# Kernel optimization log

Hardware: AMD Instinct MI355X
Metric: run time of the kernel (lower is better)

## Reference

```python
import jax, jax.numpy as jnp
import numpy as np

E, T, D_IN, D_H = 8, 2048, 2048, 5632


def setup_inputs() -> dict:
    key = jax.random.key(0)
    kx, kg, kd, ku = jax.random.split(key, 4)
    scale = 0.02  # init_std-like scaling for weights
    return {
        "x": jax.random.normal(kx, (E, T, D_IN), dtype=jnp.float32),
        "gate_proj": jax.random.normal(kg, (E, D_IN, D_H), dtype=jnp.float32) * scale,
        "down_proj": jax.random.normal(kd, (E, D_IN, D_H), dtype=jnp.float32) * scale,
        "up_proj": jax.random.normal(ku, (E, D_H, D_IN), dtype=jnp.float32) * scale,
        "tokens_per_expert": T,
    }


def reference(x, gate_proj, down_proj, up_proj, tokens_per_expert):
    # ep_size=1: dispatch/combine are identity. Grouped SwiGLU per expert.
    # x: [E, T, d_in]; gate/down: [E, d_in, d_h]; up: [E, d_h, d_in]
    g = jnp.einsum('etd,edh->eth', x, gate_proj)
    u = jnp.einsum('etd,edh->eth', x, down_proj)
    h = jax.nn.silu(g) * u  # [E, T, d_h]
    out = jnp.einsum('eth,ehd->etd', h, up_proj)  # [E, T, d_in]
    return out
```

## Files before the change

### kernel.cpp

```cpp
#include <hip/hip_runtime.h>
#include <hip/hip_bf16.h>


#define NEXP 8
#define TT   2048
#define DIN  2048
#define DH   5632
#define KP   2080

using short8 = __attribute__((ext_vector_type(8))) short;
using f32x4  = __attribute__((ext_vector_type(4))) float;

static __device__ __forceinline__ unsigned short f2bf(float f) {
    unsigned int i = __float_as_uint(f);
    return (unsigned short)((i + 0x7FFFu + ((i >> 16) & 1u)) >> 16);
}
static __device__ __forceinline__ void gld16(const void* g, void* l) {
    __builtin_amdgcn_global_load_lds(
        (const __attribute__((address_space(1))) void*)g,
        (__attribute__((address_space(3))) void*)l, 16, 0, 0);
}

__global__ __launch_bounds__(512, 2) void gemm_gu(
    const unsigned short* __restrict__ Xb,
    const unsigned short* __restrict__ Wgt,
    const unsigned short* __restrict__ Wdt,
    unsigned short* __restrict__ Hb)
{
    __shared__ __align__(16) unsigned short lds[81920];

    const int tid  = threadIdx.x;
    const int wave = tid >> 6, lane = tid & 63;
    const int l15 = lane & 15, l4 = lane >> 4;
    const int wr = wave >> 2, wc = wave & 3;

    const int bid = blockIdx.x;
    const int e   = bid & 7;
    const int cu  = bid >> 3;
    const int m0  = (cu & 7) * 256;
    const int nb  = cu >> 3;

    const unsigned short* Ae = Xb + (size_t)e * TT * KP;
    unsigned short* He = Hb + (size_t)e * TT * DH;

    const int c0 = tid, c1 = 512 + tid;
    const int cs0 = c0 ^ ((c0 >> 3) & 7), cs1 = c1 ^ ((c1 >> 3) & 7);
    const int row0 = cs0 >> 3, col0 = (cs0 & 7) * 8;
    const int row1 = cs1 >> 3, col1 = (cs1 & 7) * 8;

    int ibA[4][2], ibB[2][2];
#pragma unroll
    for (int s = 0; s < 4; ++s)
#pragma unroll
        for (int ks = 0; ks < 2; ++ks) {
            const int r = wr * 64 + s * 16 + l15;
            ibA[s][ks] = (r * 128 + ks * 64 + l4 * 16) ^ ((r & 7) << 4);
        }
#pragma unroll
    for (int s = 0; s < 2; ++s)
#pragma unroll
        for (int ks = 0; ks < 2; ++ks) {
            const int r = wc * 32 + s * 16 + l15;
            ibB[s][ks] = (r * 128 + ks * 64 + l4 * 16) ^ ((r & 7) << 4);
        }

    f32x4 acc[8][4] = {};
    short8 Aq[4][2], Gq[2][2], Dq[2][2];

    char* ldsb = (char*)lds;
    auto stageA = [&](int ro, int kk, int so) {
        gld16(Ae + (size_t)(m0 + ro + row0) * KP + (kk + col0), ldsb + so + wave * 1024);
        gld16(Ae + (size_t)(m0 + ro + row1) * KP + (kk + col1), ldsb + so + 8192 + wave * 1024);
    };
    auto stageW = [&](const unsigned short* p, int kk, int so) {
        gld16(p + (size_t)row0 * KP + (kk + col0), ldsb + so + wave * 1024);
        gld16(p + (size_t)row1 * KP + (kk + col1), ldsb + so + 8192 + wave * 1024);
    };
    auto w10 = [](int x) { return x >= 10 ? x - 10 : x; };

    const size_t NSTEP = (size_t)512 * KP;
    const unsigned short* Gc = Wgt + (size_t)e * DH * KP + (size_t)(nb * 128) * KP;
    const unsigned short* Dc = Wdt + (size_t)e * DH * KP + (size_t)(nb * 128) * KP;

    stageA(0, 0, 0 << 14);  stageW(Gc, 0, 1 << 14);  stageW(Dc, 0, 2 << 14);  stageA(128, 0, 3 << 14);
    stageA(0, 64, 4 << 14); stageW(Gc, 64, 5 << 14); stageW(Dc, 64, 6 << 14);
    asm volatile("s_waitcnt vmcnt(6)" ::: "memory");
    asm volatile("s_barrier" ::: "memory");

    const char* ldsc = (const char*)lds;
    int q = 0;
    for (int i = 0; i < 11; ++i) {
        const unsigned short* Gn = Gc + NSTEP;
        const unsigned short* Dn = Dc + NSTEP;
        for (int t = 0; t < 32; ++t) {
            const int g = (i << 5) + t;
            const int sA0 = q << 14;
            const int sG  = w10(q + 1) << 14;
            const int sD  = w10(q + 2) << 14;
            const int sA1 = w10(q + 3) << 14;
            const int stA1 = w10(q + 7) << 14;
            const int stA0 = w10(q + 8) << 14;
            const int stG  = w10(q + 9) << 14;
            const int stD  = sA0;

#pragma unroll
            for (int s = 0; s < 4; ++s) {
                Aq[s][0] = *(const short8*)(ldsc + sA0 + ibA[s][0]);
                Aq[s][1] = *(const short8*)(ldsc + sA0 + ibA[s][1]);
            }
#pragma unroll
            for (int s = 0; s < 2; ++s) {
                Gq[s][0] = *(const short8*)(ldsc + sG + ibB[s][0]);
                Gq[s][1] = *(const short8*)(ldsc + sG + ibB[s][1]);
                Dq[s][0] = *(const short8*)(ldsc + sD + ibB[s][0]);
                Dq[s][1] = *(const short8*)(ldsc + sD + ibB[s][1]);
            }
            if (i < 10 || t + 1 < 32)
                stageA(128, ((t + 1) & 31) * 64, stA1);
            asm volatile("s_waitcnt lgkmcnt(0)" ::: "memory");
            __builtin_amdgcn_sched_barrier(0);
            __builtin_amdgcn_s_setprio(1);
#pragma unroll
            for (int m = 0; m < 4; ++m)
#pragma unroll
                for (int n = 0; n < 2; ++n) {
                    acc[m][n] = __builtin_amdgcn_mfma_f32_16x16x32_bf16(Aq[m][0], Gq[n][0], acc[m][n], 0, 0, 0);
                    acc[m][n] = __builtin_amdgcn_mfma_f32_16x16x32_bf16(Aq[m][1], Gq[n][1], acc[m][n], 0, 0, 0);
                }
            __builtin_amdgcn_s_setprio(0);
            if (i < 10 || t + 2 < 32)
                stageA(0, ((t + 2) & 31) * 64, stA0);
            __builtin_amdgcn_s_setprio(1);
#pragma unroll
            for (int m = 0; m < 4; ++m)
#pragma unroll
                for (int n = 0; n < 2; ++n) {
                    acc[m][2 + n] = __builtin_amdgcn_mfma_f32_16x16x32_bf16(Aq[m][0], Dq[n][0], acc[m][2 + n], 0, 0, 0);
                    acc[m][2 + n] = __builtin_amdgcn_mfma_f32_16x16x32_bf16(Aq[m][1], Dq[n][1], acc[m][2 + n], 0, 0, 0);
                }
            __builtin_amdgcn_s_setprio(0);
#pragma unroll
            for (int s = 0; s < 4; ++s) {
                Aq[s][0] = *(const short8*)(ldsc + sA1 + ibA[s][0]);
                Aq[s][1] = *(const short8*)(ldsc + sA1 + ibA[s][1]);
            }
            if (i < 10 || t + 2 < 32)
                stageW((t + 2 < 32) ? Gc : Gn, ((t + 2) & 31) * 64, stG);
            asm volatile("s_waitcnt lgkmcnt(0)" ::: "memory");
            __builtin_amdgcn_sched_barrier(0);
            __builtin_amdgcn_s_setprio(1);
#pragma unroll
            for (int m = 0; m < 4; ++m)
#pragma unroll
                for (int n = 0; n < 2; ++n) {
                    acc[4 + m][2 + n] = __builtin_amdgcn_mfma_f32_16x16x32_bf16(Aq[m][0], Dq[n][0], acc[4 + m][2 + n], 0, 0, 0);
                    acc[4 + m][2 + n] = __builtin_amdgcn_mfma_f32_16x16x32_bf16(Aq[m][1], Dq[n][1], acc[4 + m][2 + n], 0, 0, 0);
                }
#pragma unroll
            for (int m = 0; m < 4; ++m)
#pragma unroll
                for (int n = 0; n < 2; ++n) {
                    acc[4 + m][n] = __builtin_amdgcn_mfma_f32_16x16x32_bf16(Aq[m][0], Gq[n][0], acc[4 + m][n], 0, 0, 0);
                    acc[4 + m][n] = __builtin_amdgcn_mfma_f32_16x16x32_bf16(Aq[m][1], Gq[n][1], acc[4 + m][n], 0, 0, 0);
                }
            __builtin_amdgcn_s_setprio(0);
            asm volatile("s_barrier" ::: "memory");
            if (i < 10 || t + 2 < 32)
                stageW((t + 2 < 32) ? Dc : Dn, ((t + 2) & 31) * 64, stD);
            if (g < 350)       asm volatile("s_waitcnt vmcnt(6)" ::: "memory");
            else if (g == 350) asm volatile("s_waitcnt vmcnt(0)" ::: "memory");
            asm volatile("s_barrier" ::: "memory");
            q = w10(q + 4);
        }

        const int n0i = (4 * i + nb) * 128;
#pragma unroll
        for (int fm = 0; fm < 8; ++fm) {
            const int row_b = m0 + (fm >> 2) * 128 + wr * 64 + (fm & 3) * 16 + l4 * 4;
#pragma unroll
            for (int nr = 0; nr < 2; ++nr) {
                const int col = n0i + wc * 32 + nr * 16 + l15;
#pragma unroll
                for (int j = 0; j < 4; ++j) {
                    const float gv = acc[fm][nr][j];
                    const float uv = acc[fm][2 + nr][j];
                    const float h = gv / (1.f + __expf(-gv)) * uv;
                    He[(size_t)(row_b + j) * DH + col] = f2bf(h);
                }
            }
        }
#pragma unroll
        for (int m = 0; m < 8; ++m)
#pragma unroll
            for (int n = 0; n < 4; ++n)
                acc[m][n] = (f32x4){0.f, 0.f, 0.f, 0.f};
        Gc = Gn; Dc = Dn;
    }
}

__global__ __launch_bounds__(512, 2) void gemm_out(
    const unsigned short* __restrict__ Ab,
    const unsigned short* __restrict__ Btb,
    float* __restrict__ Cf)
{
    __shared__ __align__(16) unsigned short lds[81920];

    const int tid  = threadIdx.x;
    const int wave = tid >> 6, lane = tid & 63;
    const int l15 = lane & 15, l4 = lane >> 4;
    const int wr = wave >> 2, wc = wave & 3;

    const int bid = blockIdx.x;
    const int e   = bid & 7;
    const int cu  = bid >> 3;
    const int m0  = (cu & 7) * 256;
    const int nb  = cu >> 3;

    const int N = DIN, K = DH;
    const unsigned short* Ae = Ab + (size_t)e * TT * DH;

    const int c0 = tid, c1 = 512 + tid;
    const int cs0 = c0 ^ ((c0 >> 3) & 7), cs1 = c1 ^ ((c1 >> 3) & 7);
    const int row0 = cs0 >> 3, col0 = (cs0 & 7) * 8;
    const int row1 = cs1 >> 3, col1 = (cs1 & 7) * 8;

    int ibA[4][2], ibB[2][2];
#pragma unroll
    for (int s = 0; s < 4; ++s)
#pragma unroll
        for (int ks = 0; ks < 2; ++ks) {
            const int r = wr * 64 + s * 16 + l15;
            ibA[s][ks] = (r * 128 + ks * 64 + l4 * 16) ^ ((r & 7) << 4);
        }
#pragma unroll
    for (int s = 0; s < 2; ++s)
#pragma unroll
        for (int ks = 0; ks < 2; ++ks) {
            const int r = wc * 32 + s * 16 + l15;
            ibB[s][ks] = (r * 128 + ks * 64 + l4 * 16) ^ ((r & 7) << 4);
        }

    f32x4 acc[8][4] = {};
    short8 Aq[4][2], B0q[2][2], B1q[2][2];

    char* ldsb = (char*)lds;
    auto stageA = [&](int ro, int kk, int so) {
        gld16(Ae + (size_t)(m0 + ro + row0) * K + (kk + col0), ldsb + so + wave * 1024);
        gld16(Ae + (size_t)(m0 + ro + row1) * K + (kk + col1), ldsb + so + 8192 + wave * 1024);
    };
    auto stageB = [&](const unsigned short* base, int co, int kk, int so) {
        gld16(base + (size_t)(co + row0) * K + (kk + col0), ldsb + so + wave * 1024);
        gld16(base + (size_t)(co + row1) * K + (kk + col1), ldsb + so + 8192 + wave * 1024);
    };
    auto w10 = [](int x) { return x >= 10 ? x - 10 : x; };

    const size_t NSTEP = (size_t)1024 * K;
    const unsigned short* Bc = Btb + (size_t)e * DIN * DH + (size_t)(nb * 256) * K;

    stageA(0, 0, 0 << 14); stageB(Bc, 0, 0, 1 << 14); stageB(Bc, 128, 0, 2 << 14); stageA(128, 0, 3 << 14);
    stageA(0, 64, 4 << 14); stageB(Bc, 0, 64, 5 << 14); stageB(Bc, 128, 64, 6 << 14);
    asm volatile("s_waitcnt vmcnt(6)" ::: "memory");
    asm volatile("s_barrier" ::: "memory");

    const char* ldsc = (const char*)lds;
    int q = 0;
    for (int i = 0; i < 2; ++i) {
        const unsigned short* Bn = Bc + NSTEP;
        for (int t = 0; t < 88; ++t) {
            const int g = i * 88 + t;
            const int sA0 = q << 14;
            const int sB0 = w10(q + 1) << 14;
            const int sB1 = w10(q + 2) << 14;
            const int sA1 = w10(q + 3) << 14;
            const int stA1 = w10(q + 7) << 14;
            const int stA0 = w10(q + 8) << 14;
            const int stB0 = w10(q + 9) << 14;
            const int stB1 = sA0;

#pragma unroll
            for (int s = 0; s < 4; ++s) {
                Aq[s][0] = *(const short8*)(ldsc + sA0 + ibA[s][0]);
                Aq[s][1] = *(const short8*)(ldsc + sA0 + ibA[s][1]);
            }
#pragma unroll
            for (int s = 0; s < 2; ++s) {
                B0q[s][0] = *(const short8*)(ldsc + sB0 + ibB[s][0]);
                B0q[s][1] = *(const short8*)(ldsc + sB0 + ibB[s][1]);
                B1q[s][0] = *(const short8*)(ldsc + sB1 + ibB[s][0]);
                B1q[s][1] = *(const short8*)(ldsc + sB1 + ibB[s][1]);
            }
            {
                const int tt = t + 1;
                if (i < 1 || tt < 88)
                    stageA(128, (tt >= 88 ? tt - 88 : tt) * 64, stA1);
            }
            asm volatile("s_waitcnt lgkmcnt(0)" ::: "memory");
            __builtin_amdgcn_sched_barrier(0);
            __builtin_amdgcn_s_setprio(1);
#pragma unroll
            for (int m = 0; m < 4; ++m)
#pragma unroll
                for (int n = 0; n < 2; ++n) {
                    acc[m][n] = __builtin_amdgcn_mfma_f32_16x16x32_bf16(Aq[m][0], B0q[n][0], acc[m][n], 0, 0, 0);
                    acc[m][n] = __builtin_amdgcn_mfma_f32_16x16x32_bf16(Aq[m][1], B0q[n][1], acc[m][n], 0, 0, 0);
                }
            __builtin_amdgcn_s_setprio(0);
            {
                const int tt = t + 2;
                if (i < 1 || tt < 88)
                    stageA(0, (tt >= 88 ? tt - 88 : tt) * 64, stA0);
            }
            __builtin_amdgcn_s_setprio(1);
#pragma unroll
            for (int m = 0; m < 4; ++m)
#pragma unroll
                for (int n = 0; n < 2; ++n) {
                    acc[m][2 + n] = __builtin_amdgcn_mfma_f32_16x16x32_bf16(Aq[m][0], B1q[n][0], acc[m][2 + n], 0, 0, 0);
                    acc[m][2 + n] = __builtin_amdgcn_mfma_f32_16x16x32_bf16(Aq[m][1], B1q[n][1], acc[m][2 + n], 0, 0, 0);
                }
            __builtin_amdgcn_s_setprio(0);
#pragma unroll
            for (int s = 0; s < 4; ++s) {
                Aq[s][0] = *(const short8*)(ldsc + sA1 + ibA[s][0]);
                Aq[s][1] = *(const short8*)(ldsc + sA1 + ibA[s][1]);
            }
            {
                const int tt = t + 2;
                if (i < 1 || tt < 88)
                    stageB((tt >= 88 ? Bn : Bc), 0, (tt >= 88 ? tt - 88 : tt) * 64, stB0);
            }
            asm volatile("s_waitcnt lgkmcnt(0)" ::: "memory");
            __builtin_amdgcn_sched_barrier(0);
            __builtin_amdgcn_s_setprio(1);
#pragma unroll
            for (int m = 0; m < 4; ++m)
#pragma unroll
                for (int n = 0; n < 2; ++n) {
                    acc[4 + m][2 + n] = __builtin_amdgcn_mfma_f32_16x16x32_bf16(Aq[m][0], B1q[n][0], acc[4 + m][2 + n], 0, 0, 0);
                    acc[4 + m][2 + n] = __builtin_amdgcn_mfma_f32_16x16x32_bf16(Aq[m][1], B1q[n][1], acc[4 + m][2 + n], 0, 0, 0);
                }
#pragma unroll
            for (int m = 0; m < 4; ++m)
#pragma unroll
                for (int n = 0; n < 2; ++n) {
                    acc[4 + m][n] = __builtin_amdgcn_mfma_f32_16x16x32_bf16(Aq[m][0], B0q[n][0], acc[4 + m][n], 0, 0, 0);
                    acc[4 + m][n] = __builtin_amdgcn_mfma_f32_16x16x32_bf16(Aq[m][1], B0q[n][1], acc[4 + m][n], 0, 0, 0);
                }
            __builtin_amdgcn_s_setprio(0);
            asm volatile("s_barrier" ::: "memory");
            {
                const int tt = t + 2;
                if (i < 1 || tt < 88)
                    stageB((tt >= 88 ? Bn : Bc), 128, (tt >= 88 ? tt - 88 : tt) * 64, stB1);
            }
            if (g < 174)       asm volatile("s_waitcnt vmcnt(6)" ::: "memory");
            else if (g == 174) asm volatile("s_waitcnt vmcnt(0)" ::: "memory");
            asm volatile("s_barrier" ::: "memory");
            q = w10(q + 4);
        }

        const int n0i = (4 * i + nb) * 256;
        float* Ce = Cf + (size_t)e * TT * DIN;
#pragma unroll
        for (int fm = 0; fm < 8; ++fm) {
            const int row_b = (fm >> 2) * 128 + wr * 64 + (fm & 3) * 16 + l4 * 4;
#pragma unroll
            for (int fn = 0; fn < 4; ++fn) {
                const int col = n0i + (fn >> 1) * 128 + wc * 32 + (fn & 1) * 16 + l15;
#pragma unroll
                for (int j = 0; j < 4; ++j)
                    Ce[(size_t)(m0 + row_b + j) * N + col] = acc[fm][fn][j];
            }
        }
#pragma unroll
        for (int m = 0; m < 8; ++m)
#pragma unroll
            for (int n = 0; n < 4; ++n)
                acc[m][n] = (f32x4){0.f, 0.f, 0.f, 0.f};
        Bc = Bn;
    }
}

__global__ __launch_bounds__(256) void transpose_f32_bf16(
    const float* __restrict__ in, unsigned short* __restrict__ out,
    int R, int C, int opitch, size_t ies, size_t oes)
{
    in  += (size_t)blockIdx.z * ies;
    out += (size_t)blockIdx.z * oes;
    __shared__ unsigned short t[64][65];
    const int tid = threadIdx.x;
    const int lr = tid >> 4, lc = (tid & 15) * 4;
    const int r0 = blockIdx.y * 64, c0 = blockIdx.x * 64;
#pragma unroll
    for (int i = 0; i < 4; ++i) {
        const int row = lr + i * 16;
        const float4 v = *(const float4*)(in + (size_t)(r0 + row) * C + c0 + lc);
        t[row][lc + 0] = f2bf(v.x); t[row][lc + 1] = f2bf(v.y);
        t[row][lc + 2] = f2bf(v.z); t[row][lc + 3] = f2bf(v.w);
    }
    __syncthreads();
#pragma unroll
    for (int i = 0; i < 4; ++i) {
        const int crow = lr + i * 16;
        ushort4 wv;
        wv.x = t[lc + 0][crow]; wv.y = t[lc + 1][crow];
        wv.z = t[lc + 2][crow]; wv.w = t[lc + 3][crow];
        *(ushort4*)(out + (size_t)(c0 + crow) * opitch + r0 + lc) = wv;
    }
}

__global__ __launch_bounds__(256) void conv_pad_f32_bf16(
    const float* __restrict__ in, unsigned short* __restrict__ out, int n8)
{
    int i = blockIdx.x * 256 + threadIdx.x;
    const int stride = gridDim.x * 256;
    for (; i < n8; i += stride) {
        const int row = i >> 8;
        const int col = (i & 255) * 8;
        const float4 v0 = *(const float4*)(in + (size_t)row * DIN + col);
        const float4 v1 = *(const float4*)(in + (size_t)row * DIN + col + 4);
        ushort4 a, b;
        a.x = f2bf(v0.x); a.y = f2bf(v0.y); a.z = f2bf(v0.z); a.w = f2bf(v0.w);
        b.x = f2bf(v1.x); b.y = f2bf(v1.y); b.z = f2bf(v1.z); b.w = f2bf(v1.w);
        *(ushort4*)(out + (size_t)row * KP + col) = a;
        *(ushort4*)(out + (size_t)row * KP + col + 4) = b;
    }
}

extern "C" void kernel_launch(void* const* d_in, const int* in_sizes, int n_in,
                              void* d_out, int out_size, void* d_ws, size_t ws_size,
                              hipStream_t stream)
{
    const float* x  = (const float*)d_in[0];
    const float* wg = (const float*)d_in[1];
    const float* wd = (const float*)d_in[2];
    const float* wu = (const float*)d_in[3];
    float* out = (float*)d_out;

    const size_t XSZ = (size_t)TT * KP;
    const size_t WPSZ = (size_t)DH * KP;
    const size_t WSZ = (size_t)DIN * DH;
    unsigned short* xb  = (unsigned short*)d_ws;
    unsigned short* wgt = xb  + (size_t)NEXP * XSZ;
    unsigned short* wdt = wgt + (size_t)NEXP * WPSZ;
    unsigned short* hb  = wdt + (size_t)NEXP * WPSZ;

    conv_pad_f32_bf16<<<4096, 256, 0, stream>>>(x, xb, NEXP * TT * (DIN / 8));
    transpose_f32_bf16<<<dim3(DH / 64, DIN / 64, NEXP), 256, 0, stream>>>(
        wg, wgt, DIN, DH, KP, WSZ, WPSZ);
    transpose_f32_bf16<<<dim3(DH / 64, DIN / 64, NEXP), 256, 0, stream>>>(
        wd, wdt, DIN, DH, KP, WSZ, WPSZ);
    gemm_gu<<<256, 512, 0, stream>>>(xb, wgt, wdt, hb);
    transpose_f32_bf16<<<dim3(DIN / 64, DH / 64, NEXP), 256, 0, stream>>>(
        wu, wgt, DH, DIN, DH, WSZ, WSZ);
    gemm_out<<<256, 512, 0, stream>>>(hb, wgt, out);
}
```

Baseline: 1.324 ms.

## Load weight fragments directly from global into registers, stage only activations in LDS

Both GEMM kernels stop staging the weight (B) tiles through LDS. Each wave now reads its own weight fragments straight from global memory into registers, while only the activation tile goes through a smaller triple-buffered LDS ring with a single barrier per step. This cuts LDS footprint, LDS traffic and barriers per K-step. In exchange, weight fragments are no longer shared across waves through LDS, so each weight line is fetched by several waves via cache, and global load latency is exposed unless it overlaps with the MFMAs.

```diff
diff --git a/kernel.cpp b/kernel.cpp
--- a/kernel.cpp
+++ b/kernel.cpp
@@ -27,7 +27,7 @@
     const unsigned short* __restrict__ Wdt,
     unsigned short* __restrict__ Hb)
 {
-    __shared__ __align__(16) unsigned short lds[81920];
+    __shared__ __align__(16) unsigned short lds[49152];
 
     const int tid  = threadIdx.x;
     const int wave = tid >> 6, lane = tid & 63;
@@ -40,15 +40,18 @@
     const int m0  = (cu & 7) * 256;
     const int nb  = cu >> 3;
 
-    const unsigned short* Ae = Xb + (size_t)e * TT * KP;
+    const unsigned short* Ae = Xb + (size_t)e * TT * KP + (size_t)m0 * KP;
     unsigned short* He = Hb + (size_t)e * TT * DH;
 
     const int c0 = tid, c1 = 512 + tid;
     const int cs0 = c0 ^ ((c0 >> 3) & 7), cs1 = c1 ^ ((c1 >> 3) & 7);
     const int row0 = cs0 >> 3, col0 = (cs0 & 7) * 8;
     const int row1 = cs1 >> 3, col1 = (cs1 & 7) * 8;
-
-    int ibA[4][2], ibB[2][2];
+    const size_t loff0 = (size_t)row0 * KP + col0;
+    const size_t loff1 = (size_t)row1 * KP + col1;
+    const int wvoff = wave * 1024;
+
+    int ibA[4][2];
 #pragma unroll
     for (int s = 0; s < 4; ++s)
 #pragma unroll
@@ -56,121 +59,110 @@
             const int r = wr * 64 + s * 16 + l15;
             ibA[s][ks] = (r * 128 + ks * 64 + l4 * 16) ^ ((r & 7) << 4);
         }
-#pragma unroll
-    for (int s = 0; s < 2; ++s)
-#pragma unroll
-        for (int ks = 0; ks < 2; ++ks) {
+
+    const size_t NSTEP = (size_t)512 * KP;
+    const unsigned short* gR[2];
+    const unsigned short* dR[2];
+    {
+        const unsigned short* Gb = Wgt + (size_t)e * DH * KP + (size_t)(nb * 128) * KP;
+        const unsigned short* Db = Wdt + (size_t)e * DH * KP + (size_t)(nb * 128) * KP;
+#pragma unroll
+        for (int s = 0; s < 2; ++s) {
             const int r = wc * 32 + s * 16 + l15;
-            ibB[s][ks] = (r * 128 + ks * 64 + l4 * 16) ^ ((r & 7) << 4);
-        }
+            gR[s] = Gb + (size_t)r * KP + l4 * 8;
+            dR[s] = Db + (size_t)r * KP + l4 * 8;
+        }
+    }
 
     f32x4 acc[8][4] = {};
     short8 Aq[4][2], Gq[2][2], Dq[2][2];
 
     char* ldsb = (char*)lds;
-    auto stageA = [&](int ro, int kk, int so) {
-        gld16(Ae + (size_t)(m0 + ro + row0) * KP + (kk + col0), ldsb + so + wave * 1024);
-        gld16(Ae + (size_t)(m0 + ro + row1) * KP + (kk + col1), ldsb + so + 8192 + wave * 1024);
+    const char* ldsc = (const char*)lds;
+    auto stageA2 = [&](int kk, int so) {
+        gld16(Ae + kk + loff0, ldsb + so + wvoff);
+        gld16(Ae + kk + loff1, ldsb + so + 8192 + wvoff);
+        gld16(Ae + (size_t)128 * KP + kk + loff0, ldsb + so + 16384 + wvoff);
+        gld16(Ae + (size_t)128 * KP + kk + loff1, ldsb + so + 16384 + 8192 + wvoff);
     };
-    auto stageW = [&](const unsigned short* p, int kk, int so) {
-        gld16(p + (size_t)row0 * KP + (kk + col0), ldsb + so + wave * 1024);
-        gld16(p + (size_t)row1 * KP + (kk + col1), ldsb + so + 8192 + wave * 1024);
-    };
-    auto w10 = [](int x) { return x >= 10 ? x - 10 : x; };
-
-    const size_t NSTEP = (size_t)512 * KP;
-    const unsigned short* Gc = Wgt + (size_t)e * DH * KP + (size_t)(nb * 128) * KP;
-    const unsigned short* Dc = Wdt + (size_t)e * DH * KP + (size_t)(nb * 128) * KP;
-
-    stageA(0, 0, 0 << 14);  stageW(Gc, 0, 1 << 14);  stageW(Dc, 0, 2 << 14);  stageA(128, 0, 3 << 14);
-    stageA(0, 64, 4 << 14); stageW(Gc, 64, 5 << 14); stageW(Dc, 64, 6 << 14);
-    asm volatile("s_waitcnt vmcnt(6)" ::: "memory");
+
+    stageA2(0, 0);
+    stageA2(64, 32768);
+    asm volatile("s_waitcnt vmcnt(4)" ::: "memory");
     asm volatile("s_barrier" ::: "memory");
 
-    const char* ldsc = (const char*)lds;
-    int q = 0;
+    int u = 0;
     for (int i = 0; i < 11; ++i) {
-        const unsigned short* Gn = Gc + NSTEP;
-        const unsigned short* Dn = Dc + NSTEP;
         for (int t = 0; t < 32; ++t) {
-            const int g = (i << 5) + t;
-            const int sA0 = q << 14;
-            const int sG  = w10(q + 1) << 14;
-            const int sD  = w10(q + 2) << 14;
-            const int sA1 = w10(q + 3) << 14;
-            const int stA1 = w10(q + 7) << 14;
-            const int stA0 = w10(q + 8) << 14;
-            const int stG  = w10(q + 9) << 14;
-            const int stD  = sA0;
+            const int sb = u << 15;
+            const int u2 = (u >= 1) ? u - 1 : u + 2;
+            const int kb = t * 64;
+
+#pragma unroll
+            for (int s = 0; s < 2; ++s)
+#pragma unroll
+                for (int ks = 0; ks < 2; ++ks) {
+                    Gq[s][ks] = *(const short8*)(gR[s] + kb + ks * 32);
+                    Dq[s][ks] = *(const short8*)(dR[s] + kb + ks * 32);
+                }
+
+            const bool st = (i < 10) || (t + 2 < 32);
+            if (st) stageA2(((t + 2) & 31) * 64, u2 << 15);
 
 #pragma unroll
             for (int s = 0; s < 4; ++s) {
-                Aq[s][0] = *(const short8*)(ldsc + sA0 + ibA[s][0]);
-                Aq[s][1] = *(const short8*)(ldsc + sA0 + ibA[s][1]);
-            }
-#pragma unroll
-            for (int s = 0; s < 2; ++s) {
-                Gq[s][0] = *(const short8*)(ldsc + sG + ibB[s][0]);
-                Gq[s][1] = *(const short8*)(ldsc + sG + ibB[s][1]);
-                Dq[s][0] = *(const short8*)(ldsc + sD + ibB[s][0]);
-                Dq[s][1] = *(const short8*)(ldsc + sD + ibB[s][1]);
-            }
-            if (i < 10 || t + 1 < 32)
-                stageA(128, ((t + 1) & 31) * 64, stA1);
+                Aq[s][0] = *(const short8*)(ldsc + sb + ibA[s][0]);
+                Aq[s][1] = *(const short8*)(ldsc + sb + ibA[s][1]);
+            }
+
+            if (st) asm volatile("s_waitcnt vmcnt(4)" ::: "memory");
+            else    asm volatile("s_waitcnt vmcnt(0)" ::: "memory");
+            __builtin_amdgcn_sched_barrier(0);
+
+            __builtin_amdgcn_s_setprio(1);
+#pragma unroll
+            for (int m = 0; m < 4; ++m)
+#pragma unroll
+                for (int n = 0; n < 2; ++n) {
+                    acc[m][n] = __builtin_amdgcn_mfma_f32_16x16x32_bf16(Aq[m][0], Gq[n][0], acc[m][n], 0, 0, 0);
+                    acc[m][n] = __builtin_amdgcn_mfma_f32_16x16x32_bf16(Aq[m][1], Gq[n][1], acc[m][n], 0, 0, 0);
+                }
+#pragma unroll
+            for (int m = 0; m < 4; ++m)
+#pragma unroll
+                for (int n = 0; n < 2; ++n) {
+                    acc[m][2 + n] = __builtin_amdgcn_mfma_f32_16x16x32_bf16(Aq[m][0], Dq[n][0], acc[m][2 + n], 0, 0, 0);
+                    acc[m][2 + n] = __builtin_amdgcn_mfma_f32_16x16x32_bf16(Aq[m][1], Dq[n][1], acc[m][2 + n], 0, 0, 0);
+                }
+            __builtin_amdgcn_s_setprio(0);
+
+#pragma unroll
+            for (int s = 0; s < 4; ++s) {
+                Aq[s][0] = *(const short8*)(ldsc + sb + 16384 + ibA[s][0]);
+                Aq[s][1] = *(const short8*)(ldsc + sb + 16384 + ibA[s][1]);
+            }
+
+            __builtin_amdgcn_s_setprio(1);
+#pragma unroll
+            for (int m = 0; m < 4; ++m)
+#pragma unroll
+                for (int n = 0; n < 2; ++n) {
+                    acc[4 + m][2 + n] = __builtin_amdgcn_mfma_f32_16x16x32_bf16(Aq[m][0], Dq[n][0], acc[4 + m][2 + n], 0, 0, 0);
+                    acc[4 + m][2 + n] = __builtin_amdgcn_mfma_f32_16x16x32_bf16(Aq[m][1], Dq[n][1], acc[4 + m][2 + n], 0, 0, 0);
+                }
+#pragma unroll
+            for (int m = 0; m < 4; ++m)
+#pragma unroll
+                for (int n = 0; n < 2; ++n) {
+                    acc[4 + m][n] = __builtin_amdgcn_mfma_f32_16x16x32_bf16(Aq[m][0], Gq[n][0], acc[4 + m][n], 0, 0, 0);
+                    acc[4 + m][n] = __builtin_amdgcn_mfma_f32_16x16x32_bf16(Aq[m][1], Gq[n][1], acc[4 + m][n], 0, 0, 0);
+                }
+            __builtin_amdgcn_s_setprio(0);
+
             asm volatile("s_waitcnt lgkmcnt(0)" ::: "memory");
             __builtin_amdgcn_sched_barrier(0);
-            __builtin_amdgcn_s_setprio(1);
-#pragma unroll
-            for (int m = 0; m < 4; ++m)
-#pragma unroll
-                for (int n = 0; n < 2; ++n) {
-                    acc[m][n] = __builtin_amdgcn_mfma_f32_16x16x32_bf16(Aq[m][0], Gq[n][0], acc[m][n], 0, 0, 0);
-                    acc[m][n] = __builtin_amdgcn_mfma_f32_16x16x32_bf16(Aq[m][1], Gq[n][1], acc[m][n], 0, 0, 0);
-                }
-            __builtin_amdgcn_s_setprio(0);
-            if (i < 10 || t + 2 < 32)
-                stageA(0, ((t + 2) & 31) * 64, stA0);
-            __builtin_amdgcn_s_setprio(1);
-#pragma unroll
-            for (int m = 0; m < 4; ++m)
-#pragma unroll
-                for (int n = 0; n < 2; ++n) {
-                    acc[m][2 + n] = __builtin_amdgcn_mfma_f32_16x16x32_bf16(Aq[m][0], Dq[n][0], acc[m][2 + n], 0, 0, 0);
-                    acc[m][2 + n] = __builtin_amdgcn_mfma_f32_16x16x32_bf16(Aq[m][1], Dq[n][1], acc[m][2 + n], 0, 0, 0);
-                }
-            __builtin_amdgcn_s_setprio(0);
-#pragma unroll
-            for (int s = 0; s < 4; ++s) {
-                Aq[s][0] = *(const short8*)(ldsc + sA1 + ibA[s][0]);
-                Aq[s][1] = *(const short8*)(ldsc + sA1 + ibA[s][1]);
-            }
-            if (i < 10 || t + 2 < 32)
-                stageW((t + 2 < 32) ? Gc : Gn, ((t + 2) & 31) * 64, stG);
-            asm volatile("s_waitcnt lgkmcnt(0)" ::: "memory");
-            __builtin_amdgcn_sched_barrier(0);
-            __builtin_amdgcn_s_setprio(1);
-#pragma unroll
-            for (int m = 0; m < 4; ++m)
-#pragma unroll
-                for (int n = 0; n < 2; ++n) {
-                    acc[4 + m][2 + n] = __builtin_amdgcn_mfma_f32_16x16x32_bf16(Aq[m][0], Dq[n][0], acc[4 + m][2 + n], 0, 0, 0);
-                    acc[4 + m][2 + n] = __builtin_amdgcn_mfma_f32_16x16x32_bf16(Aq[m][1], Dq[n][1], acc[4 + m][2 + n], 0, 0, 0);
-                }
-#pragma unroll
-            for (int m = 0; m < 4; ++m)
-#pragma unroll
-                for (int n = 0; n < 2; ++n) {
-                    acc[4 + m][n] = __builtin_amdgcn_mfma_f32_16x16x32_bf16(Aq[m][0], Gq[n][0], acc[4 + m][n], 0, 0, 0);
-                    acc[4 + m][n] = __builtin_amdgcn_mfma_f32_16x16x32_bf16(Aq[m][1], Gq[n][1], acc[4 + m][n], 0, 0, 0);
-                }
-            __builtin_amdgcn_s_setprio(0);
             asm volatile("s_barrier" ::: "memory");
-            if (i < 10 || t + 2 < 32)
-                stageW((t + 2 < 32) ? Dc : Dn, ((t + 2) & 31) * 64, stD);
-            if (g < 350)       asm volatile("s_waitcnt vmcnt(6)" ::: "memory");
-            else if (g == 350) asm volatile("s_waitcnt vmcnt(0)" ::: "memory");
-            asm volatile("s_barrier" ::: "memory");
-            q = w10(q + 4);
+            u = (u >= 2) ? 0 : u + 1;
         }
 
         const int n0i = (4 * i + nb) * 128;
@@ -194,7 +186,8 @@
 #pragma unroll
             for (int n = 0; n < 4; ++n)
                 acc[m][n] = (f32x4){0.f, 0.f, 0.f, 0.f};
-        Gc = Gn; Dc = Dn;
+#pragma unroll
+        for (int s = 0; s < 2; ++s) { gR[s] += NSTEP; dR[s] += NSTEP; }
     }
 }
 
@@ -203,7 +196,7 @@
     const unsigned short* __restrict__ Btb,
     float* __restrict__ Cf)
 {
-    __shared__ __align__(16) unsigned short lds[81920];
+    __shared__ __align__(16) unsigned short lds[49152];
 
     const int tid  = threadIdx.x;
     const int wave = tid >> 6, lane = tid & 63;
@@ -216,15 +209,17 @@
     const int m0  = (cu & 7) * 256;
     const int nb  = cu >> 3;
 
-    const int N = DIN, K = DH;
-    const unsigned short* Ae = Ab + (size_t)e * TT * DH;
+    const unsigned short* Ae = Ab + (size_t)e * TT * DH + (size_t)m0 * DH;
 
     const int c0 = tid, c1 = 512 + tid;
     const int cs0 = c0 ^ ((c0 >> 3) & 7), cs1 = c1 ^ ((c1 >> 3) & 7);
     const int row0 = cs0 >> 3, col0 = (cs0 & 7) * 8;
     const int row1 = cs1 >> 3, col1 = (cs1 & 7) * 8;
-
-    int ibA[4][2], ibB[2][2];
+    const size_t loff0 = (size_t)row0 * DH + col0;
+    const size_t loff1 = (size_t)row1 * DH + col1;
+    const int wvoff = wave * 1024;
+
+    int ibA[4][2];
 #pragma unroll
     for (int s = 0; s < 4; ++s)
 #pragma unroll
@@ -232,131 +227,112 @@
             const int r = wr * 64 + s * 16 + l15;
             ibA[s][ks] = (r * 128 + ks * 64 + l4 * 16) ^ ((r & 7) << 4);
         }
-#pragma unroll
-    for (int s = 0; s < 2; ++s)
-#pragma unroll
-        for (int ks = 0; ks < 2; ++ks) {
+
+    const size_t NSTEP = (size_t)1024 * DH;
+    const unsigned short* b0R[2];
+    const unsigned short* b1R[2];
+    {
+        const unsigned short* Bb = Btb + (size_t)e * DIN * DH + (size_t)(nb * 256) * DH;
+#pragma unroll
+        for (int s = 0; s < 2; ++s) {
             const int r = wc * 32 + s * 16 + l15;
-            ibB[s][ks] = (r * 128 + ks * 64 + l4 * 16) ^ ((r & 7) << 4);
-        }
+            b0R[s] = Bb + (size_t)r * DH + l4 * 8;
+            b1R[s] = b0R[s] + (size_t)128 * DH;
+        }
+    }
 
     f32x4 acc[8][4] = {};
     short8 Aq[4][2], B0q[2][2], B1q[2][2];
 
     char* ldsb = (char*)lds;
-    auto stageA = [&](int ro, int kk, int so) {
-        gld16(Ae + (size_t)(m0 + ro + row0) * K + (kk + col0), ldsb + so + wave * 1024);
-        gld16(Ae + (size_t)(m0 + ro + row1) * K + (kk + col1), ldsb + so + 8192 + wave * 1024);
+    const char* ldsc = (const char*)lds;
+    auto stageA2 = [&](int kk, int so) {
+        gld16(Ae + kk + loff0, ldsb + so + wvoff);
+        gld16(Ae + kk + loff1, ldsb + so + 8192 + wvoff);
+        gld16(Ae + (size_t)128 * DH + kk + loff0, ldsb + so + 16384 + wvoff);
+        gld16(Ae + (size_t)128 * DH + kk + loff1, ldsb + so + 16384 + 8192 + wvoff);
     };
-    auto stageB = [&](const unsigned short* base, int co, int kk, int so) {
-        gld16(base + (size_t)(co + row0) * K + (kk + col0), ldsb + so + wave * 1024);
-        gld16(base + (size_t)(co + row1) * K + (kk + col1), ldsb + so + 8192 + wave * 1024);
-    };
-    auto w10 = [](int x) { return x >= 10 ? x - 10 : x; };
-
-    const size_t NSTEP = (size_t)1024 * K;
-    const unsigned short* Bc = Btb + (size_t)e * DIN * DH + (size_t)(nb * 256) * K;
-
-    stageA(0, 0, 0 << 14); stageB(Bc, 0, 0, 1 << 14); stageB(Bc, 128, 0, 2 << 14); stageA(128, 0, 3 << 14);
-    stageA(0, 64, 4 << 14); stageB(Bc, 0, 64, 5 << 14); stageB(Bc, 128, 64, 6 << 14);
-    asm volatile("s_waitcnt vmcnt(6)" ::: "memory");
+
+    stageA2(0, 0);
+    stageA2(64, 32768);
+    asm volatile("s_waitcnt vmcnt(4)" ::: "memory");
     asm volatile("s_barrier" ::: "memory");
 
-    const char* ldsc = (const char*)lds;
-    int q = 0;
+    int u = 0;
     for (int i = 0; i < 2; ++i) {
-        const unsigned short* Bn = Bc + NSTEP;
         for (int t = 0; t < 88; ++t) {
-            const int g = i * 88 + t;
-            const int sA0 = q << 14;
-            const int sB0 = w10(q + 1) << 14;
-            const int sB1 = w10(q + 2) << 14;
-            const int sA1 = w10(q + 3) << 14;
-            const int stA1 = w10(q + 7) << 14;
-            const int stA0 = w10(q + 8) << 14;
-            const int stB0 = w10(q + 9) << 14;
-            const int stB1 = sA0;
+            const int sb = u << 15;
+            const int u2 = (u >= 1) ? u - 1 : u + 2;
+            const int kb = t * 64;
+
+#pragma unroll
+            for (int s = 0; s < 2; ++s)
+#pragma unroll
+                for (int ks = 0; ks < 2; ++ks) {
+                    B0q[s][ks] = *(const short8*)(b0R[s] + kb + ks * 32);
+                    B1q[s][ks] = *(const short8*)(b1R[s] + kb + ks * 32);
+                }
+
+            const bool st = (i < 1) || (t + 2 < 88);
+            if (st) {
+                const int t2 = (t + 2 >= 88) ? t + 2 - 88 : t + 2;
+                stageA2(t2 * 64, u2 << 15);
+            }
 
 #pragma unroll
             for (int s = 0; s < 4; ++s) {
-                Aq[s][0] = *(const short8*)(ldsc + sA0 + ibA[s][0]);
-                Aq[s][1] = *(const short8*)(ldsc + sA0 + ibA[s][1]);
-            }
-#pragma unroll
-            for (int s = 0; s < 2; ++s) {
-                B0q[s][0] = *(const short8*)(ldsc + sB0 + ibB[s][0]);
-                B0q[s][1] = *(const short8*)(ldsc + sB0 + ibB[s][1]);
-                B1q[s][0] = *(const short8*)(ldsc + sB1 + ibB[s][0]);
-                B1q[s][1] = *(const short8*)(ldsc + sB1 + ibB[s][1]);
-            }
-            {
-                const int tt = t + 1;
-                if (i < 1 || tt < 88)
-                    stageA(128, (tt >= 88 ? tt - 88 : tt) * 64, stA1);
-            }
+                Aq[s][0] = *(const short8*)(ldsc + sb + ibA[s][0]);
+                Aq[s][1] = *(const short8*)(ldsc + sb + ibA[s][1]);
+            }
+
+            if (st) asm volatile("s_waitcnt vmcnt(4)" ::: "memory");
+            else    asm volatile("s_waitcnt vmcnt(0)" ::: "memory");
+            __builtin_amdgcn_sched_barrier(0);
+
+            __builtin_amdgcn_s_setprio(1);
+#pragma unroll
+            for (int m = 0; m < 4; ++m)
+#pragma unroll
+                for (int n = 0; n < 2; ++n) {
+                    acc[m][n] = __builtin_amdgcn_mfma_f32_16x16x32_bf16(Aq[m][0], B0q[n][0], acc[m][n], 0, 0, 0);
+                    acc[m][n] = __builtin_amdgcn_mfma_f32_16x16x32_bf16(Aq[m][1], B0q[n][1], acc[m][n], 0, 0, 0);
+                }
+#pragma unroll
+            for (int m = 0; m < 4; ++m)
+#pragma unroll
+                for (int n = 0; n < 2; ++n) {
+                    acc[m][2 + n] = __builtin_amdgcn_mfma_f32_16x16x32_bf16(Aq[m][0], B1q[n][0], acc[m][2 + n], 0, 0, 0);
+                    acc[m][2 + n] = __builtin_amdgcn_mfma_f32_16x16x32_bf16(Aq[m][1], B1q[n][1], acc[m][2 + n], 0, 0, 0);
+                }
+            __builtin_amdgcn_s_setprio(0);
+
+#pragma unroll
+            for (int s = 0; s < 4; ++s) {
+                Aq[s][0] = *(const short8*)(ldsc + sb + 16384 + ibA[s][0]);
+                Aq[s][1] = *(const short8*)(ldsc + sb + 16384 + ibA[s][1]);
+            }
+
+            __builtin_amdgcn_s_setprio(1);
+#pragma unroll
+            for (int m = 0; m < 4; ++m)
+#pragma unroll
+                for (int n = 0; n < 2; ++n) {
+                    acc[4 + m][2 + n] = __builtin_amdgcn_mfma_f32_16x16x32_bf16(Aq[m][0], B1q[n][0], acc[4 + m][2 + n], 0, 0, 0);
+                    acc[4 + m][2 + n] = __builtin_amdgcn_mfma_f32_16x16x32_bf16(Aq[m][1], B1q[n][1], acc[4 + m][2 + n], 0, 0, 0);
+                }
+#pragma unroll
+            for (int m = 0; m < 4; ++m)
+#pragma unroll
+                for (int n = 0; n < 2; ++n) {
+                    acc[4 + m][n] = __builtin_amdgcn_mfma_f32_16x16x32_bf16(Aq[m][0], B0q[n][0], acc[4 + m][n], 0, 0, 0);
+                    acc[4 + m][n] = __builtin_amdgcn_mfma_f32_16x16x32_bf16(Aq[m][1], B0q[n][1], acc[4 + m][n], 0, 0, 0);
+                }
+            __builtin_amdgcn_s_setprio(0);
+
             asm volatile("s_waitcnt lgkmcnt(0)" ::: "memory");
             __builtin_amdgcn_sched_barrier(0);
-            __builtin_amdgcn_s_setprio(1);
-#pragma unroll
-            for (int m = 0; m < 4; ++m)
-#pragma unroll
-                for (int n = 0; n < 2; ++n) {
-                    acc[m][n] = __builtin_amdgcn_mfma_f32_16x16x32_bf16(Aq[m][0], B0q[n][0], acc[m][n], 0, 0, 0);
-                    acc[m][n] = __builtin_amdgcn_mfma_f32_16x16x32_bf16(Aq[m][1], B0q[n][1], acc[m][n], 0, 0, 0);
-                }
-            __builtin_amdgcn_s_setprio(0);
-            {
-                const int tt = t + 2;
-                if (i < 1 || tt < 88)
-                    stageA(0, (tt >= 88 ? tt - 88 : tt) * 64, stA0);
-            }
-            __builtin_amdgcn_s_setprio(1);
-#pragma unroll
-            for (int m = 0; m < 4; ++m)
-#pragma unroll
-                for (int n = 0; n < 2; ++n) {
-                    acc[m][2 + n] = __builtin_amdgcn_mfma_f32_16x16x32_bf16(Aq[m][0], B1q[n][0], acc[m][2 + n], 0, 0, 0);
-                    acc[m][2 + n] = __builtin_amdgcn_mfma_f32_16x16x32_bf16(Aq[m][1], B1q[n][1], acc[m][2 + n], 0, 0, 0);
-                }
-            __builtin_amdgcn_s_setprio(0);
-#pragma unroll
-            for (int s = 0; s < 4; ++s) {
-                Aq[s][0] = *(const short8*)(ldsc + sA1 + ibA[s][0]);
-                Aq[s][1] = *(const short8*)(ldsc + sA1 + ibA[s][1]);
-            }
-            {
-                const int tt = t + 2;
-                if (i < 1 || tt < 88)
-                    stageB((tt >= 88 ? Bn : Bc), 0, (tt >= 88 ? tt - 88 : tt) * 64, stB0);
-            }
-            asm volatile("s_waitcnt lgkmcnt(0)" ::: "memory");
-            __builtin_amdgcn_sched_barrier(0);
-            __builtin_amdgcn_s_setprio(1);
-#pragma unroll
-            for (int m = 0; m < 4; ++m)
-#pragma unroll
-                for (int n = 0; n < 2; ++n) {
-                    acc[4 + m][2 + n] = __builtin_amdgcn_mfma_f32_16x16x32_bf16(Aq[m][0], B1q[n][0], acc[4 + m][2 + n], 0, 0, 0);
-                    acc[4 + m][2 + n] = __builtin_amdgcn_mfma_f32_16x16x32_bf16(Aq[m][1], B1q[n][1], acc[4 + m][2 + n], 0, 0, 0);
-                }
-#pragma unroll
-            for (int m = 0; m < 4; ++m)
-#pragma unroll
-                for (int n = 0; n < 2; ++n) {
-                    acc[4 + m][n] = __builtin_amdgcn_mfma_f32_16x16x32_bf16(Aq[m][0], B0q[n][0], acc[4 + m][n], 0, 0, 0);
-                    acc[4 + m][n] = __builtin_amdgcn_mfma_f32_16x16x32_bf16(Aq[m][1], B0q[n][1], acc[4 + m][n], 0, 0, 0);
-                }
-            __builtin_amdgcn_s_setprio(0);
             asm volatile("s_barrier" ::: "memory");
-            {
-                const int tt = t + 2;
-                if (i < 1 || tt < 88)
-                    stageB((tt >= 88 ? Bn : Bc), 128, (tt >= 88 ? tt - 88 : tt) * 64, stB1);
-            }
-            if (g < 174)       asm volatile("s_waitcnt vmcnt(6)" ::: "memory");
-            else if (g == 174) asm volatile("s_waitcnt vmcnt(0)" ::: "memory");
-            asm volatile("s_barrier" ::: "memory");
-            q = w10(q + 4);
+            u = (u >= 2) ? 0 : u + 1;
         }
 
         const int n0i = (4 * i + nb) * 256;
@@ -369,7 +345,7 @@
                 const int col = n0i + (fn >> 1) * 128 + wc * 32 + (fn & 1) * 16 + l15;
 #pragma unroll
                 for (int j = 0; j < 4; ++j)
-                    Ce[(size_t)(m0 + row_b + j) * N + col] = acc[fm][fn][j];
+                    Ce[(size_t)(m0 + row_b + j) * DIN + col] = acc[fm][fn][j];
             }
         }
 #pragma unroll
@@ -377,7 +353,8 @@
 #pragma unroll
             for (int n = 0; n < 4; ++n)
                 acc[m][n] = (f32x4){0.f, 0.f, 0.f, 0.f};
-        Bc = Bn;
+#pragma unroll
+        for (int s = 0; s < 2; ++s) { b0R[s] += NSTEP; b1R[s] += NSTEP; }
     }
 }
 
```

Result: slower. 1.946 ms (+46.9%).
